# Kernel optimization log

Measured on AMD Instinct MI355X. Metric: run time of the kernel, lower is better.

The kernel has to match this reference:

```python
import jax, jax.numpy as jnp
import numpy as np

DIM = 1024
NB = 25            # num_basis_functions
ALPHA_X = 1.0
DT = 0.001
MAX_TIME = 10.0
TAU = 1.0
ALPHA_Y = 25.0
BETA_Y = 6.25
WEIGHT_SCALE = 1000.0
T = int(MAX_TIME / DT) + 1   # rollout buffer length = 10001


def setup_inputs() -> dict:
    key = jax.random.key(0)
    k1, k2, k3 = jax.random.split(key, 3)
    y0 = jax.random.normal(k1, (DIM,), dtype=jnp.float32)
    # learned parameters of the module
    g = jax.random.normal(k2, (DIM,), dtype=jnp.float32)
    weights = jax.random.normal(k3, (DIM, NB), dtype=jnp.float32) / NB
    return {"y0": y0, "g": g, "weights": weights}


def reference(y0, g, weights):
    # basis function centers / widths (canonical system)
    c = jnp.exp(-ALPHA_X * jnp.linspace(0.0, MAX_TIME, NB)).astype(y0.dtype)
    h = (NB / c).astype(y0.dtype)
    decay = jnp.asarray(1.0 - ALPHA_X * TAU * DT, y0.dtype)

    def step(carry, _):
        x, y, dy = carry
        x = x * decay                                   # decay_time()
        psi = jnp.exp(-h * (x - c) ** 2)                # [NB]
        # force(y0): sum over basis functions, per dim
        force = (WEIGHT_SCALE * (weights @ psi)) * x * (g - y0) / jnp.sum(psi)  # [DIM]
        ddy = ALPHA_Y * (BETA_Y * (g - y) - dy) + force
        ndy = dy + TAU * DT * ddy
        ny = y + TAU * DT * ndy
        return (x, ny, ndy), jnp.concatenate([ny, ndy])

    x0 = jnp.asarray(1.0, y0.dtype)
    dy0 = jnp.zeros_like(y0)
    _, rows = jax.lax.scan(step, (x0, y0, dy0), None, length=T - 1)  # [T-1, 2*DIM]
    first = jnp.concatenate([y0, dy0])[None]                          # [1, 2*DIM]
    ydy = jnp.concatenate([first, rows], axis=0)                      # [T, 2*DIM]
    y0rep = jnp.broadcast_to(y0, (T, DIM))
    return jnp.concatenate([y0rep, ydy], axis=1)                      # [T, 3*DIM]
```

## Files before the change

kernel.cpp:

```cpp
#include <hip/hip_runtime.h>
#include <math.h>


#define DIM    1024
#define NB     25
#define NSTEP  10000
#define CHUNKS 100
#define LSTEPS 100
#define QS     32

__global__ void k_tables(float* __restrict__ q) {
    int t0 = blockIdx.x * blockDim.x + threadIdx.x;
    if (t0 >= NSTEP) return;
    int t = t0 + 1;
    const float decay = 1.0f - 1.0f * 1.0f * 0.001f;
    float x = (float)exp((double)t * log((double)decay));
    float psi[NB];
    float S = 0.f;
#pragma unroll
    for (int k = 0; k < NB; ++k) {
        float lk = (10.0f / 24.0f) * (float)k;
        float ck = expf(-lk);
        float hk = 25.0f / ck;
        float dxc = x - ck;
        float p = expf(-hk * dxc * dxc);
        psi[k] = p;
        S += p;
    }
    float scale = 1000.0f * x / S;
#pragma unroll
    for (int k = 0; k < NB; ++k) q[t0 * QS + k] = psi[k] * scale;
#pragma unroll
    for (int k = NB; k < QS; ++k) q[t0 * QS + k] = 0.f;
}

__global__ __launch_bounds__(256) void k_phase1(const float* __restrict__ q,
                                                const float* __restrict__ W,
                                                const float* __restrict__ g,
                                                const float* __restrict__ y0,
                                                float* __restrict__ r) {
    const int c = blockIdx.y;
    const int d = blockIdx.x * 256 + threadIdx.x;
    float w[NB];
#pragma unroll
    for (int k = 0; k < NB; ++k) w[k] = W[d * NB + k];
    const float gd  = g[d];
    const float gd0 = gd - y0[d];
    float y = 0.f, dy = 0.f;
    const float* qp = q + (size_t)c * LSTEPS * QS;
#pragma unroll 4
    for (int j = 0; j < LSTEPS; ++j) {
        float dot = 0.f;
#pragma unroll
        for (int k = 0; k < NB; ++k) dot += w[k] * qp[k];
        qp += QS;
        float f   = dot * gd0;
        float ddy = 25.0f * (6.25f * (gd - y) - dy) + f;
        dy = dy + 0.001f * ddy;
        y  = y + 0.001f * dy;
    }
    r[c * DIM + d] = y;
    r[CHUNKS * DIM + c * DIM + d] = dy;
}

__global__ void k_phase2(const float* __restrict__ r,
                         const float* __restrict__ y0,
                         float* __restrict__ vs,
                         double m00, double m01, double m10, double m11) {
    const int d = blockIdx.x * blockDim.x + threadIdx.x;
    double vy = (double)y0[d], vdy = 0.0;
    float ry = r[d], rdy = r[CHUNKS * DIM + d];
    for (int c = 0; c < CHUNKS; ++c) {
        vs[c * DIM + d] = (float)vy;
        vs[CHUNKS * DIM + c * DIM + d] = (float)vdy;
        float ry_n = 0.f, rdy_n = 0.f;
        if (c + 1 < CHUNKS) {
            ry_n  = r[(c + 1) * DIM + d];
            rdy_n = r[(CHUNKS + c + 1) * DIM + d];
        }
        double ny  = m00 * vy + m01 * vdy + (double)ry;
        double ndy = m10 * vy + m11 * vdy + (double)rdy;
        vy = ny; vdy = ndy;
        ry = ry_n; rdy = rdy_n;
    }
}

__global__ __launch_bounds__(256) void k_phase3(const float* __restrict__ q,
                                                const float* __restrict__ W,
                                                const float* __restrict__ g,
                                                const float* __restrict__ y0,
                                                const float* __restrict__ vs,
                                                float* __restrict__ out) {
    const int c = blockIdx.y;
    const int d = blockIdx.x * 256 + threadIdx.x;
    float w[NB];
#pragma unroll
    for (int k = 0; k < NB; ++k) w[k] = W[d * NB + k];
    const float y0d = y0[d];
    const float gd  = g[d];
    const float gd0 = gd - y0d;
    float y  = vs[c * DIM + d];
    float dy = vs[CHUNKS * DIM + c * DIM + d];
    if (c == 0) {
        out[d] = y0d;
        out[DIM + d] = y0d;
        out[2 * DIM + d] = 0.f;
    }
    const float* qp = q + (size_t)c * LSTEPS * QS;
    float* op = out + (size_t)(c * LSTEPS + 1) * (3 * DIM);
#pragma unroll 4
    for (int j = 0; j < LSTEPS; ++j) {
        float dot = 0.f;
#pragma unroll
        for (int k = 0; k < NB; ++k) dot += w[k] * qp[k];
        qp += QS;
        float f   = dot * gd0;
        float ddy = 25.0f * (6.25f * (gd - y) - dy) + f;
        dy = dy + 0.001f * ddy;
        y  = y + 0.001f * dy;
        op[d] = y0d;
        op[DIM + d] = y;
        op[2 * DIM + d] = dy;
        op += 3 * DIM;
    }
}

extern "C" void kernel_launch(void* const* d_in, const int* in_sizes, int n_in,
                              void* d_out, int out_size, void* d_ws, size_t ws_size,
                              hipStream_t stream) {
    const float* y0 = (const float*)d_in[0];
    const float* g  = (const float*)d_in[1];
    const float* W  = (const float*)d_in[2];
    float* out = (float*)d_out;

    float* q  = (float*)d_ws;
    float* r  = q  + (size_t)NSTEP * QS;
    float* vs = r  + (size_t)2 * CHUNKS * DIM;

    const double dtD = (double)0.001f;
    const double aD = 25.0, bD = 6.25;
    const double a00 = 1.0 - dtD * dtD * aD * bD;
    const double a01 = dtD * (1.0 - dtD * aD);
    const double a10 = -dtD * aD * bD;
    const double a11 = 1.0 - dtD * aD;
    double m00 = 1, m01 = 0, m10 = 0, m11 = 1;
    for (int i = 0; i < LSTEPS; ++i) {
        double t00 = a00 * m00 + a01 * m10;
        double t01 = a00 * m01 + a01 * m11;
        double t10 = a10 * m00 + a11 * m10;
        double t11 = a10 * m01 + a11 * m11;
        m00 = t00; m01 = t01; m10 = t10; m11 = t11;
    }

    k_tables<<<(NSTEP + 255) / 256, 256, 0, stream>>>(q);
    k_phase1<<<dim3(DIM / 256, CHUNKS), 256, 0, stream>>>(q, W, g, y0, r);
    k_phase2<<<DIM / 256, 256, 0, stream>>>(r, y0, vs, m00, m01, m10, m11);
    k_phase3<<<dim3(DIM / 256, CHUNKS), 256, 0, stream>>>(q, W, g, y0, vs, out);
}
```

Measured before the change: 180.0 us.

## Replace per-chunk phase-1 rollout with precomputed linear-response projections

Exploits linearity of the dynamics: the forcing impulse response over a chunk is folded into per-chunk basis tables QY/QD, so computing each chunk's zero-state contribution becomes a 25-term dot product instead of a 100-step simulation. Chunks shrink to 50 steps with 200 chunks, and the scan and rollout kernels run with 64-thread blocks to raise block-level parallelism. The scan stages per-dim chunk data in shared memory, and the output buffer is reused as scratch for the dots. This adds a longer serial scan and some rounding differences from the projected sums.

Result: faster. 163.5 us (-9.2%).

```diff
diff --git a/kernel.cpp b/kernel.cpp
--- a/kernel.cpp
+++ b/kernel.cpp
@@ -5,94 +5,113 @@
 #define DIM    1024
 #define NB     25
 #define NSTEP  10000
-#define CHUNKS 100
-#define LSTEPS 100
+#define CHUNKS 200
+#define LSTEPS 50
 #define QS     32
 
-__global__ void k_tables(float* __restrict__ q) {
-    int t0 = blockIdx.x * blockDim.x + threadIdx.x;
-    if (t0 >= NSTEP) return;
-    int t = t0 + 1;
-    const float decay = 1.0f - 1.0f * 1.0f * 0.001f;
-    float x = (float)exp((double)t * log((double)decay));
-    float psi[NB];
-    float S = 0.f;
+__global__ __launch_bounds__(64) void k_prep(float* __restrict__ q,
+                                             float* __restrict__ QY,
+                                             float* __restrict__ QD,
+                                             double logdecay,
+                                             double a00, double a01,
+                                             double a10, double a11) {
+    __shared__ float lq[LSTEPS][NB + 1];
+    const int c = blockIdx.x;
+    const int tid = threadIdx.x;
+    if (tid < LSTEPS) {
+        int t = c * LSTEPS + tid + 1;
+        float x = (float)exp((double)t * logdecay);
+        float psi[NB];
+        float S = 0.f;
+#pragma unroll
+        for (int k = 0; k < NB; ++k) {
+            float lk = (10.0f / 24.0f) * (float)k;
+            float ck = expf(-lk);
+            float hk = 25.0f / ck;
+            float dxc = x - ck;
+            float p = expf(-hk * dxc * dxc);
+            psi[k] = p;
+            S += p;
+        }
+        float scale = 1000.0f * x / S;
+        float* qrow = q + (size_t)(c * LSTEPS + tid) * QS;
+#pragma unroll
+        for (int k = 0; k < NB; ++k) {
+            float v = psi[k] * scale;
+            qrow[k] = v;
+            lq[tid][k] = v;
+        }
+    }
+    __syncthreads();
+    if (tid < NB) {
+        double py = (double)0.001f * (double)0.001f;
+        double pd = (double)0.001f;
+        double qy = 0.0, qd = 0.0;
+        for (int j = LSTEPS - 1; j >= 0; --j) {
+            double v = (double)lq[j][tid];
+            qy += py * v;
+            qd += pd * v;
+            double npy = a00 * py + a01 * pd;
+            double npd = a10 * py + a11 * pd;
+            py = npy; pd = npd;
+        }
+        QY[c * QS + tid] = (float)qy;
+        QD[c * QS + tid] = (float)qd;
+    }
+}
+
+__global__ __launch_bounds__(256) void k_dots(const float* __restrict__ QY,
+                                              const float* __restrict__ QD,
+                                              const float* __restrict__ W,
+                                              const float* __restrict__ g,
+                                              const float* __restrict__ y0,
+                                              float* __restrict__ dots,
+                                              double spY, double spD) {
+    const int c = blockIdx.y;
+    const int d = blockIdx.x * 256 + threadIdx.x;
+    const float gd  = g[d];
+    const float gd0 = gd - y0[d];
+    float sy = 0.f, sd = 0.f;
 #pragma unroll
     for (int k = 0; k < NB; ++k) {
-        float lk = (10.0f / 24.0f) * (float)k;
-        float ck = expf(-lk);
-        float hk = 25.0f / ck;
-        float dxc = x - ck;
-        float p = expf(-hk * dxc * dxc);
-        psi[k] = p;
-        S += p;
+        float wk = W[d * NB + k];
+        sy += wk * QY[c * QS + k];
+        sd += wk * QD[c * QS + k];
     }
-    float scale = 1000.0f * x / S;
-#pragma unroll
-    for (int k = 0; k < NB; ++k) q[t0 * QS + k] = psi[k] * scale;
-#pragma unroll
-    for (int k = NB; k < QS; ++k) q[t0 * QS + k] = 0.f;
+    dots[c * DIM + d]                = (float)((double)gd * spY + (double)gd0 * (double)sy);
+    dots[CHUNKS * DIM + c * DIM + d] = (float)((double)gd * spD + (double)gd0 * (double)sd);
 }
 
-__global__ __launch_bounds__(256) void k_phase1(const float* __restrict__ q,
-                                                const float* __restrict__ W,
-                                                const float* __restrict__ g,
-                                                const float* __restrict__ y0,
-                                                float* __restrict__ r) {
-    const int c = blockIdx.y;
-    const int d = blockIdx.x * 256 + threadIdx.x;
-    float w[NB];
-#pragma unroll
-    for (int k = 0; k < NB; ++k) w[k] = W[d * NB + k];
-    const float gd  = g[d];
-    const float gd0 = gd - y0[d];
-    float y = 0.f, dy = 0.f;
-    const float* qp = q + (size_t)c * LSTEPS * QS;
-#pragma unroll 4
-    for (int j = 0; j < LSTEPS; ++j) {
-        float dot = 0.f;
-#pragma unroll
-        for (int k = 0; k < NB; ++k) dot += w[k] * qp[k];
-        qp += QS;
-        float f   = dot * gd0;
-        float ddy = 25.0f * (6.25f * (gd - y) - dy) + f;
-        dy = dy + 0.001f * ddy;
-        y  = y + 0.001f * dy;
+__global__ __launch_bounds__(64) void k_scan(const float* __restrict__ dots,
+                                             const float* __restrict__ y0,
+                                             float* __restrict__ vs,
+                                             double m00, double m01,
+                                             double m10, double m11) {
+    __shared__ float ls[CHUNKS][2][64];
+    const int tid = threadIdx.x;
+    const int d = blockIdx.x * 64 + tid;
+    for (int c = 0; c < CHUNKS; ++c) {
+        ls[c][0][tid] = dots[c * DIM + d];
+        ls[c][1][tid] = dots[CHUNKS * DIM + c * DIM + d];
     }
-    r[c * DIM + d] = y;
-    r[CHUNKS * DIM + c * DIM + d] = dy;
-}
-
-__global__ void k_phase2(const float* __restrict__ r,
-                         const float* __restrict__ y0,
-                         float* __restrict__ vs,
-                         double m00, double m01, double m10, double m11) {
-    const int d = blockIdx.x * blockDim.x + threadIdx.x;
     double vy = (double)y0[d], vdy = 0.0;
-    float ry = r[d], rdy = r[CHUNKS * DIM + d];
     for (int c = 0; c < CHUNKS; ++c) {
         vs[c * DIM + d] = (float)vy;
         vs[CHUNKS * DIM + c * DIM + d] = (float)vdy;
-        float ry_n = 0.f, rdy_n = 0.f;
-        if (c + 1 < CHUNKS) {
-            ry_n  = r[(c + 1) * DIM + d];
-            rdy_n = r[(CHUNKS + c + 1) * DIM + d];
-        }
-        double ny  = m00 * vy + m01 * vdy + (double)ry;
-        double ndy = m10 * vy + m11 * vdy + (double)rdy;
+        double ny  = m00 * vy + m01 * vdy + (double)ls[c][0][tid];
+        double ndy = m10 * vy + m11 * vdy + (double)ls[c][1][tid];
         vy = ny; vdy = ndy;
-        ry = ry_n; rdy = rdy_n;
     }
 }
 
-__global__ __launch_bounds__(256) void k_phase3(const float* __restrict__ q,
-                                                const float* __restrict__ W,
-                                                const float* __restrict__ g,
-                                                const float* __restrict__ y0,
-                                                const float* __restrict__ vs,
-                                                float* __restrict__ out) {
+__global__ __launch_bounds__(64) void k_roll(const float* __restrict__ q,
+                                             const float* __restrict__ W,
+                                             const float* __restrict__ g,
+                                             const float* __restrict__ y0,
+                                             const float* __restrict__ vs,
+                                             float* __restrict__ out) {
     const int c = blockIdx.y;
-    const int d = blockIdx.x * 256 + threadIdx.x;
+    const int d = blockIdx.x * 64 + threadIdx.x;
     float w[NB];
 #pragma unroll
     for (int k = 0; k < NB; ++k) w[k] = W[d * NB + k];
@@ -108,7 +127,7 @@
     }
     const float* qp = q + (size_t)c * LSTEPS * QS;
     float* op = out + (size_t)(c * LSTEPS + 1) * (3 * DIM);
-#pragma unroll 4
+#pragma unroll 2
     for (int j = 0; j < LSTEPS; ++j) {
         float dot = 0.f;
 #pragma unroll
@@ -134,26 +153,36 @@
     float* out = (float*)d_out;
 
     float* q  = (float*)d_ws;
-    float* r  = q  + (size_t)NSTEP * QS;
-    float* vs = r  + (size_t)2 * CHUNKS * DIM;
+    float* QY = q  + (size_t)NSTEP * QS;
+    float* QD = QY + (size_t)CHUNKS * QS;
+    float* vs = QD + (size_t)CHUNKS * QS;
+    float* dots = out;
 
     const double dtD = (double)0.001f;
-    const double aD = 25.0, bD = 6.25;
-    const double a00 = 1.0 - dtD * dtD * aD * bD;
+    const double aD = 25.0, abD = 25.0 * 6.25;
+    const double a00 = 1.0 - dtD * dtD * abD;
     const double a01 = dtD * (1.0 - dtD * aD);
-    const double a10 = -dtD * aD * bD;
+    const double a10 = -dtD * abD;
     const double a11 = 1.0 - dtD * aD;
     double m00 = 1, m01 = 0, m10 = 0, m11 = 1;
+    double py = dtD * dtD, pd = dtD, sY = 0.0, sD = 0.0;
     for (int i = 0; i < LSTEPS; ++i) {
         double t00 = a00 * m00 + a01 * m10;
         double t01 = a00 * m01 + a01 * m11;
         double t10 = a10 * m00 + a11 * m10;
         double t11 = a10 * m01 + a11 * m11;
         m00 = t00; m01 = t01; m10 = t10; m11 = t11;
+        sY += py; sD += pd;
+        double npy = a00 * py + a01 * pd;
+        double npd = a10 * py + a11 * pd;
+        py = npy; pd = npd;
     }
+    const double spY = 156.25 * sY;
+    const double spD = 156.25 * sD;
+    const double logdecay = log((double)(1.0f - 0.001f));
 
-    k_tables<<<(NSTEP + 255) / 256, 256, 0, stream>>>(q);
-    k_phase1<<<dim3(DIM / 256, CHUNKS), 256, 0, stream>>>(q, W, g, y0, r);
-    k_phase2<<<DIM / 256, 256, 0, stream>>>(r, y0, vs, m00, m01, m10, m11);
-    k_phase3<<<dim3(DIM / 256, CHUNKS), 256, 0, stream>>>(q, W, g, y0, vs, out);
+    k_prep<<<CHUNKS, 64, 0, stream>>>(q, QY, QD, logdecay, a00, a01, a10, a11);
+    k_dots<<<dim3(DIM / 256, CHUNKS), 256, 0, stream>>>(QY, QD, W, g, y0, dots, spY, spD);
+    k_scan<<<DIM / 64, 64, 0, stream>>>(dots, y0, vs, m00, m01, m10, m11);
+    k_roll<<<dim3(DIM / 64, CHUNKS), 64, 0, stream>>>(q, W, g, y0, vs, out);
 }
```
